# Optimization experiments

Hardware: AMD Instinct MI355X
Metric: run time of the kernel (lower is better)

Reference implementation:

```python
import jax, jax.numpy as jnp
import numpy as np

B, N, D, H, E = 4, 1024, 1024, 2048, 8

def setup_inputs() -> dict:
    key = jax.random.key(0)
    ks = jax.random.split(key, 5)
    return {
        "x": jax.random.normal(ks[0], (B, N, D), dtype=jnp.float32),
        "gate_w": jax.random.normal(ks[1], (D, E), dtype=jnp.float32) * 0.02,
        "gate_b": jnp.zeros((E,), dtype=jnp.float32),
        "w1": jax.random.normal(ks[2], (E, D, H), dtype=jnp.float32) * 0.02,
        "b1": jnp.zeros((E, H), dtype=jnp.float32),
        "w2": jax.random.normal(ks[3], (E, H, D), dtype=jnp.float32) * 0.02,
        "b2": jnp.zeros((E, D), dtype=jnp.float32),
        "gamma": jnp.ones((D,), dtype=jnp.float32),
    }

def reference(x, gate_w, gate_b, w1, b1, w2, b2, gamma):
    b, n, d = x.shape
    e = w1.shape[0]
    xf = x.reshape(b * n, d)                                    # [T, D]
    # gate: softmax over experts, then top-1
    probs = jax.nn.softmax(xf @ gate_w + gate_b, axis=-1)       # [T, E]
    top_val = jnp.max(probs, axis=-1, keepdims=True)            # [T, 1]
    top_idx = jnp.argmax(probs, axis=-1)                        # [T]
    # all-expert FFN (dense reference for masked dispatch; dropout in eval)
    h = jax.nn.gelu(jnp.einsum('td,edh->eth', xf, w1) + b1[:, None, :],
                    approximate=False)                          # [E, T, H]
    eo = jnp.einsum('eth,ehd->etd', h, w2) + b2[:, None, :]     # [E, T, D]
    onehot = jax.nn.one_hot(top_idx, e, dtype=xf.dtype)         # [T, E]
    out = jnp.einsum('etd,te->td', eo, onehot)                  # select routed expert
    y = (xf + out * top_val).reshape(b, n, d)
    # RMSNorm: F.normalize (L2, eps=1e-12) * gamma * sqrt(dim)
    nrm = jnp.linalg.norm(y, axis=-1, keepdims=True)
    y = y / jnp.maximum(nrm, 1e-12) * gamma * np.float32(np.sqrt(d))
    # load-balancing loss (unbiased variance like torch.var)
    importance = probs.sum(axis=0)                              # [E]
    load_loss = jnp.var(importance, ddof=1) / (jnp.mean(importance) ** 2 + 1e-10)
    return jax.nn.gelu(y, approximate=False), load_loss
```

## Files before the change

### kernel.cpp

```cpp
#include <hip/hip_runtime.h>
#include <math.h>

#define T_TOK 4096
#define DIM   1024
#define HID   2048
#define NE    8
#define TMM   128
#define TNN   128
#define BK    64
#define GATE_BLOCKS (T_TOK / 4)

typedef unsigned int  u32;
typedef unsigned short u16;
typedef __attribute__((ext_vector_type(8))) short bf16x8;
typedef __attribute__((ext_vector_type(4))) float f32x4;

__device__ __forceinline__ float gelu_exact(float v) {
    return 0.5f * v * (1.0f + erff(v * 0.70710678118654752440f));
}

__device__ __forceinline__ float gelu_fast(float x) {
    float u = 1.5957691216057308f * (x + 0.044715f * x * x * x);
    float e = __expf(u);
    float t = 1.f - 2.f / (e + 1.f);
    return 0.5f * x * (1.f + t);
}

__device__ __forceinline__ u16 f2bf(float v) {
    u32 u = __float_as_uint(v);
    u32 r = (u + 0x7FFFu + ((u >> 16) & 1u)) >> 16;
    return (u16)r;
}

__device__ __forceinline__ void gld_lds16(const void* g, void* l) {
    __builtin_amdgcn_global_load_lds(
        (const __attribute__((address_space(1))) u32*)g,
        (__attribute__((address_space(3))) u32*)l,
        16, 0, 0);
}

__global__ __launch_bounds__(256) void gate_kernel(
    const float* __restrict__ x, const float* __restrict__ gw,
    const float* __restrict__ gb, float* __restrict__ top_val,
    int* __restrict__ top_idx, float* __restrict__ partial_imp,
    int* __restrict__ partial_cnt)
{
    __shared__ float s_imp[NE];
    __shared__ int   s_cnt[NE];
    if (threadIdx.x < NE) { s_imp[threadIdx.x] = 0.f; s_cnt[threadIdx.x] = 0; }
    __syncthreads();

    const int wave = threadIdx.x >> 6;
    const int lane = threadIdx.x & 63;
    const int t = blockIdx.x * 4 + wave;

    float acc[NE];
    #pragma unroll
    for (int e = 0; e < NE; e++) acc[e] = 0.f;

    const float* xr = x + (size_t)t * DIM;
    #pragma unroll 4
    for (int k = lane; k < DIM; k += 64) {
        float xv = xr[k];
        const float* g = gw + (size_t)k * NE;
        float4 g0 = *(const float4*)g;
        float4 g1 = *(const float4*)(g + 4);
        acc[0] += xv * g0.x; acc[1] += xv * g0.y;
        acc[2] += xv * g0.z; acc[3] += xv * g0.w;
        acc[4] += xv * g1.x; acc[5] += xv * g1.y;
        acc[6] += xv * g1.z; acc[7] += xv * g1.w;
    }
    #pragma unroll
    for (int e = 0; e < NE; e++) {
        #pragma unroll
        for (int off = 32; off > 0; off >>= 1)
            acc[e] += __shfl_down(acc[e], off, 64);
    }
    if (lane == 0) {
        float l[NE];
        float m = -1e30f;
        #pragma unroll
        for (int e = 0; e < NE; e++) { l[e] = acc[e] + gb[e]; m = fmaxf(m, l[e]); }
        float s = 0.f;
        #pragma unroll
        for (int e = 0; e < NE; e++) { l[e] = expf(l[e] - m); s += l[e]; }
        float inv = 1.f / s;
        int bi = 0; float bv = -1.f;
        #pragma unroll
        for (int e = 0; e < NE; e++) {
            float p = l[e] * inv;
            atomicAdd(&s_imp[e], p);
            if (p > bv) { bv = p; bi = e; }
        }
        top_val[t] = bv;
        top_idx[t] = bi;
        atomicAdd(&s_cnt[bi], 1);
    }
    __syncthreads();
    if (threadIdx.x < NE) {
        partial_imp[blockIdx.x * NE + threadIdx.x] = s_imp[threadIdx.x];
        partial_cnt[blockIdx.x * NE + threadIdx.x] = s_cnt[threadIdx.x];
    }
}

__global__ __launch_bounds__(256) void plan_kernel(
    const float* __restrict__ partial_imp, const int* __restrict__ partial_cnt,
    int* __restrict__ counts, int* __restrict__ offsets,
    int* __restrict__ tile_e, int* __restrict__ tile_s,
    int* __restrict__ tile_rows, int* __restrict__ ntiles,
    float* __restrict__ loss_out)
{
    __shared__ float rimp[32][NE];
    __shared__ int   rcnt[32][NE];
    const int th = threadIdx.x;
    const int e = th & 7, chunk = th >> 3;
    float si = 0.f; int sc = 0;
    #pragma unroll 8
    for (int i = 0; i < GATE_BLOCKS / 32; i++) {
        const int b = chunk * (GATE_BLOCKS / 32) + i;
        si += partial_imp[b * NE + e];
        sc += partial_cnt[b * NE + e];
    }
    rimp[chunk][e] = si;
    rcnt[chunk][e] = sc;
    __syncthreads();
    if (th < NE) {
        float s = 0.f; int c = 0;
        for (int i = 0; i < 32; i++) { s += rimp[i][th]; c += rcnt[i][th]; }
        counts[th] = c;
        rimp[0][th] = s;
        rcnt[0][th] = c;
    }
    __syncthreads();
    if (th == 0) {
        int off = 0, nt = 0;
        for (int ee = 0; ee < NE; ee++) {
            offsets[ee] = off;
            const int c = rcnt[0][ee];
            for (int s = 0; s < c; s += TMM) {
                tile_e[nt] = ee;
                tile_s[nt] = off + s;
                tile_rows[nt] = min(TMM, c - s);
                nt++;
            }
            off += c;
        }
        offsets[NE] = off;
        *ntiles = nt;

        float mean = 0.f;
        for (int ee = 0; ee < NE; ee++) mean += rimp[0][ee];
        mean *= (1.0f / NE);
        float var = 0.f;
        for (int ee = 0; ee < NE; ee++) { float d = rimp[0][ee] - mean; var += d * d; }
        var *= (1.0f / (NE - 1));
        loss_out[0] = var / (mean * mean + 1e-10f);
    }
}

__global__ __launch_bounds__(256) void scatter_kernel(
    const int* __restrict__ top_idx, const int* __restrict__ offsets,
    int* __restrict__ cursors, int* __restrict__ sorted_tok)
{
    __shared__ int lcnt[NE], lbase[NE];
    if (threadIdx.x < NE) lcnt[threadIdx.x] = 0;
    __syncthreads();
    const int t = blockIdx.x * blockDim.x + threadIdx.x;
    const int e = top_idx[t];
    const int lrank = atomicAdd(&lcnt[e], 1);
    __syncthreads();
    if (threadIdx.x < NE)
        lbase[threadIdx.x] = atomicAdd(&cursors[threadIdx.x], lcnt[threadIdx.x]);
    __syncthreads();
    sorted_tok[offsets[e] + lbase[e] + lrank] = t;
}

__global__ __launch_bounds__(256) void gather_x_kernel(
    const float* __restrict__ x, const int* __restrict__ sorted_tok,
    u16* __restrict__ xs)
{
    const int s = blockIdx.x;
    const int tok = sorted_tok[s];
    const float* src = x + (size_t)tok * DIM;
    u16* dst = xs + (size_t)s * DIM;
    const int i = threadIdx.x * 4;
    float4 v = *(const float4*)&src[i];
    ushort4 o;
    o.x = f2bf(v.x); o.y = f2bf(v.y); o.z = f2bf(v.z); o.w = f2bf(v.w);
    *(ushort4*)&dst[i] = o;
}

__global__ __launch_bounds__(256) void transpose_bf16_kernel(
    const float* __restrict__ in, u16* __restrict__ out, int R, int C)
{
    __shared__ float tile[64][65];
    const float* src = in  + (size_t)blockIdx.z * R * C;
    u16*         dst = out + (size_t)blockIdx.z * R * C;
    const int c0 = blockIdx.x * 64, r0 = blockIdx.y * 64;
    const int th = threadIdx.x;

    const int tr  = th >> 4;
    const int tc4 = (th & 15) * 4;
    #pragma unroll
    for (int i = 0; i < 4; i++) {
        const int r = tr + i * 16;
        float4 v = *(const float4*)&src[(size_t)(r0 + r) * C + c0 + tc4];
        tile[r][tc4 + 0] = v.x; tile[r][tc4 + 1] = v.y;
        tile[r][tc4 + 2] = v.z; tile[r][tc4 + 3] = v.w;
    }
    __syncthreads();
    const int cc  = th >> 4;
    const int rr4 = (th & 15) * 4;
    #pragma unroll
    for (int i = 0; i < 4; i++) {
        const int c = cc + i * 16;
        ushort4 o;
        o.x = f2bf(tile[rr4 + 0][c]);
        o.y = f2bf(tile[rr4 + 1][c]);
        o.z = f2bf(tile[rr4 + 2][c]);
        o.w = f2bf(tile[rr4 + 3][c]);
        *(ushort4*)&dst[(size_t)(c0 + c) * R + r0 + rr4] = o;
    }
}

__global__ __launch_bounds__(256) void ffn1_mfma(
    const u16* __restrict__ xs, const u16* __restrict__ w1t,
    const float* __restrict__ b1,
    const int* __restrict__ tile_e, const int* __restrict__ tile_s,
    const int* __restrict__ tile_rows, const int* __restrict__ ntiles,
    u16* __restrict__ h_buf)
{
    const int tile = blockIdx.x;
    if (tile >= *ntiles) return;
    const int e     = tile_e[tile];
    const int sbase = tile_s[tile];
    const int rows  = tile_rows[tile];
    const int nbase = blockIdx.y * TNN;

    __shared__ __align__(16) u16 As[TMM * BK];
    __shared__ __align__(16) u16 Bs[TNN * BK];

    const int th = threadIdx.x;
    const int w  = th >> 6;
    const int l  = th & 63;
    const int wm = w >> 1, wn = w & 1;
    const int lr = l >> 3;
    const int lcs = ((l & 7) ^ lr) * 8;

    const u16* aptr[4];
    #pragma unroll
    for (int c = 0; c < 4; c++) {
        int srow = sbase + w * 32 + c * 8 + lr;
        if (srow > T_TOK - 1) srow = T_TOK - 1;
        aptr[c] = xs + (size_t)srow * DIM + lcs;
    }
    const u16* wb = w1t + (size_t)e * HID * DIM + (size_t)nbase * DIM;
    const u16* bptr[4];
    #pragma unroll
    for (int c = 0; c < 4; c++)
        bptr[c] = wb + (size_t)(w * 32 + c * 8 + lr) * DIM + lcs;

    f32x4 acc[4][4] = {};

    for (int k0 = 0; k0 < DIM; k0 += BK) {
        __syncthreads();
        #pragma unroll
        for (int c = 0; c < 4; c++)
            gld_lds16(aptr[c] + k0, &As[(w * 32 + c * 8) * BK]);
        #pragma unroll
        for (int c = 0; c < 4; c++)
            gld_lds16(bptr[c] + k0, &Bs[(w * 32 + c * 8) * BK]);
        __syncthreads();
        #pragma unroll
        for (int ks = 0; ks < 2; ks++) {
            const int ko = ((ks * 4 + (l >> 4)) ^ (l & 7)) * 8;
            bf16x8 af[4], bfr[4];
            #pragma unroll
            for (int i = 0; i < 4; i++)
                af[i]  = *(const bf16x8*)&As[(wm * 64 + i * 16 + (l & 15)) * BK + ko];
            #pragma unroll
            for (int i = 0; i < 4; i++)
                bfr[i] = *(const bf16x8*)&Bs[(wn * 64 + i * 16 + (l & 15)) * BK + ko];
            #pragma unroll
            for (int mi = 0; mi < 4; mi++)
                #pragma unroll
                for (int ni = 0; ni < 4; ni++)
                    acc[mi][ni] = __builtin_amdgcn_mfma_f32_16x16x32_bf16(
                        af[mi], bfr[ni], acc[mi][ni], 0, 0, 0);
        }
    }

    const int col = l & 15, quad = l >> 4;
    #pragma unroll
    for (int ni = 0; ni < 4; ni++) {
        const int n = nbase + wn * 64 + ni * 16 + col;
        const float bias = b1[e * HID + n];
        #pragma unroll
        for (int mi = 0; mi < 4; mi++) {
            #pragma unroll
            for (int r = 0; r < 4; r++) {
                const int m = wm * 64 + mi * 16 + quad * 4 + r;
                if (m < rows) {
                    float v = acc[mi][ni][r] + bias;
                    h_buf[(size_t)(sbase + m) * HID + n] = f2bf(gelu_fast(v));
                }
            }
        }
    }
}

__global__ __launch_bounds__(256) void ffn2_mfma(
    const u16* __restrict__ h_buf, const u16* __restrict__ w2t,
    const float* __restrict__ b2, const float* __restrict__ x,
    const int* __restrict__ sorted_tok, const float* __restrict__ top_val,
    const int* __restrict__ tile_e, const int* __restrict__ tile_s,
    const int* __restrict__ tile_rows, const int* __restrict__ ntiles,
    float* __restrict__ yout)
{
    const int tile = blockIdx.x;
    if (tile >= *ntiles) return;
    const int e     = tile_e[tile];
    const int sbase = tile_s[tile];
    const int rows  = tile_rows[tile];
    const int nbase = blockIdx.y * TNN;

    __shared__ __align__(16) u16 As[TMM * BK];
    __shared__ __align__(16) u16 Bs[TNN * BK];

    const int th = threadIdx.x;
    const int w  = th >> 6;
    const int l  = th & 63;
    const int wm = w >> 1, wn = w & 1;
    const int lr = l >> 3;
    const int lcs = ((l & 7) ^ lr) * 8;

    const u16* aptr[4];
    #pragma unroll
    for (int c = 0; c < 4; c++) {
        int srow = sbase + w * 32 + c * 8 + lr;
        if (srow > T_TOK - 1) srow = T_TOK - 1;
        aptr[c] = h_buf + (size_t)srow * HID + lcs;
    }
    const u16* wb = w2t + (size_t)e * DIM * HID + (size_t)nbase * HID;
    const u16* bptr[4];
    #pragma unroll
    for (int c = 0; c < 4; c++)
        bptr[c] = wb + (size_t)(w * 32 + c * 8 + lr) * HID + lcs;

    f32x4 acc[4][4] = {};

    for (int k0 = 0; k0 < HID; k0 += BK) {
        __syncthreads();
        #pragma unroll
        for (int c = 0; c < 4; c++)
            gld_lds16(aptr[c] + k0, &As[(w * 32 + c * 8) * BK]);
        #pragma unroll
        for (int c = 0; c < 4; c++)
            gld_lds16(bptr[c] + k0, &Bs[(w * 32 + c * 8) * BK]);
        __syncthreads();
        #pragma unroll
        for (int ks = 0; ks < 2; ks++) {
            const int ko = ((ks * 4 + (l >> 4)) ^ (l & 7)) * 8;
            bf16x8 af[4], bfr[4];
            #pragma unroll
            for (int i = 0; i < 4; i++)
                af[i]  = *(const bf16x8*)&As[(wm * 64 + i * 16 + (l & 15)) * BK + ko];
            #pragma unroll
            for (int i = 0; i < 4; i++)
                bfr[i] = *(const bf16x8*)&Bs[(wn * 64 + i * 16 + (l & 15)) * BK + ko];
            #pragma unroll
            for (int mi = 0; mi < 4; mi++)
                #pragma unroll
                for (int ni = 0; ni < 4; ni++)
                    acc[mi][ni] = __builtin_amdgcn_mfma_f32_16x16x32_bf16(
                        af[mi], bfr[ni], acc[mi][ni], 0, 0, 0);
        }
    }

    const int col = l & 15, quad = l >> 4;
    float bias[4];
    #pragma unroll
    for (int ni = 0; ni < 4; ni++)
        bias[ni] = b2[e * DIM + nbase + wn * 64 + ni * 16 + col];

    #pragma unroll
    for (int mi = 0; mi < 4; mi++) {
        #pragma unroll
        for (int r = 0; r < 4; r++) {
            const int m = wm * 64 + mi * 16 + quad * 4 + r;
            if (m < rows) {
                const int t = sorted_tok[sbase + m];
                const float tv = top_val[t];
                #pragma unroll
                for (int ni = 0; ni < 4; ni++) {
                    const int n = nbase + wn * 64 + ni * 16 + col;
                    float v = acc[mi][ni][r] + bias[ni];
                    yout[(size_t)t * DIM + n] = x[(size_t)t * DIM + n] + v * tv;
                }
            }
        }
    }
}

__global__ __launch_bounds__(256) void norm_kernel(float* __restrict__ y,
                                                   const float* __restrict__ gamma)
{
    const int t = blockIdx.x;
    float* row = y + (size_t)t * DIM;
    const int th = threadIdx.x;
    float4 v = *(const float4*)&row[th * 4];
    float ss = v.x * v.x + v.y * v.y + v.z * v.z + v.w * v.w;

    const int lane = th & 63, wave = th >> 6;
    #pragma unroll
    for (int off = 32; off > 0; off >>= 1) ss += __shfl_down(ss, off, 64);
    __shared__ float red[4];
    if (lane == 0) red[wave] = ss;
    __syncthreads();
    float total = red[0] + red[1] + red[2] + red[3];

    float nrm = sqrtf(total);
    float scale = 32.0f / fmaxf(nrm, 1e-12f);

    float4 g = *(const float4*)&gamma[th * 4];
    float4 o;
    o.x = gelu_exact(v.x * scale * g.x);
    o.y = gelu_exact(v.y * scale * g.y);
    o.z = gelu_exact(v.z * scale * g.z);
    o.w = gelu_exact(v.w * scale * g.w);
    *(float4*)&row[th * 4] = o;
}

extern "C" void kernel_launch(void* const* d_in, const int* in_sizes, int n_in,
                              void* d_out, int out_size, void* d_ws, size_t ws_size,
                              hipStream_t stream) {
    const float* x      = (const float*)d_in[0];
    const float* gate_w = (const float*)d_in[1];
    const float* gate_b = (const float*)d_in[2];
    const float* w1     = (const float*)d_in[3];
    const float* b1     = (const float*)d_in[4];
    const float* w2     = (const float*)d_in[5];
    const float* b2     = (const float*)d_in[6];
    const float* gamma  = (const float*)d_in[7];

    float* out  = (float*)d_out;
    float* loss = out + (size_t)T_TOK * DIM;

    char* ws = (char*)d_ws;
    float* top_val     = (float*)(ws + 0);
    int*   top_idx     = (int*)  (ws + 16384);
    int*   sorted_tok  = (int*)  (ws + 32768);
    int*   counts      = (int*)  (ws + 49152);
    int*   cursors     = (int*)  (ws + 49216);
    int*   offsets     = (int*)  (ws + 49280);
    int*   tile_e      = (int*)  (ws + 49664);
    int*   tile_s      = (int*)  (ws + 50176);
    int*   tile_rows   = (int*)  (ws + 50688);
    int*   ntiles      = (int*)  (ws + 51200);
    float* partial_imp = (float*)(ws + 65536);
    int*   partial_cnt = (int*)  (ws + 98304);
    u16*   x_sorted    = (u16*)  (ws + 131072);
    u16*   h_buf       = (u16*)  (ws + 131072 + 8388608);
    u16*   w1t         = (u16*)  (ws + 131072 + 8388608 + 16777216);
    u16*   w2t         = (u16*)  (ws + 131072 + 8388608 + 16777216 + 33554432);

    hipMemsetAsync(ws + 49216, 0, 64, stream);

    gate_kernel<<<GATE_BLOCKS, 256, 0, stream>>>(x, gate_w, gate_b, top_val,
                                                 top_idx, partial_imp,
                                                 partial_cnt);
    plan_kernel<<<1, 256, 0, stream>>>(partial_imp, partial_cnt, counts,
                                       offsets, tile_e, tile_s, tile_rows,
                                       ntiles, loss);
    scatter_kernel<<<T_TOK / 256, 256, 0, stream>>>(top_idx, offsets, cursors,
                                                    sorted_tok);
    gather_x_kernel<<<T_TOK, 256, 0, stream>>>(x, sorted_tok, x_sorted);
    transpose_bf16_kernel<<<dim3(HID / 64, DIM / 64, NE), 256, 0, stream>>>(
        w1, w1t, DIM, HID);
    transpose_bf16_kernel<<<dim3(DIM / 64, HID / 64, NE), 256, 0, stream>>>(
        w2, w2t, HID, DIM);

    ffn1_mfma<<<dim3(40, HID / TNN), 256, 0, stream>>>(
        x_sorted, w1t, b1, tile_e, tile_s, tile_rows, ntiles, h_buf);
    ffn2_mfma<<<dim3(40, DIM / TNN), 256, 0, stream>>>(
        h_buf, w2t, b2, x, sorted_tok, top_val, tile_e, tile_s, tile_rows,
        ntiles, out);
    norm_kernel<<<T_TOK, 256, 0, stream>>>(out, gamma);
}
```

Baseline: 320.6 us.

## Fuse weight transposes into gate kernel and widen FFN1 tiles to 128x256

Merges the two weight-transpose kernels and the gate kernel into one prep launch, so independent work shares a single grid and two launches go away. FFN1 now uses 512-thread blocks covering 256 output columns, doubling reuse of the A tile per load. Both FFN grids are reordered so blockIdx.x walks N tiles and blockIdx.y walks token tiles, which groups blocks that share the same expert weights and activations in time. The larger FFN1 block uses more LDS and registers per block, which may lower occupancy.

```diff
diff --git a/kernel.cpp b/kernel.cpp
--- a/kernel.cpp
+++ b/kernel.cpp
@@ -6,7 +6,6 @@
 #define HID   2048
 #define NE    8
 #define TMM   128
-#define TNN   128
 #define BK    64
 #define GATE_BLOCKS (T_TOK / 4)
 
@@ -39,20 +38,69 @@
         16, 0, 0);
 }
 
-__global__ __launch_bounds__(256) void gate_kernel(
+__device__ __forceinline__ void transpose_body(
+    const float* __restrict__ in, u16* __restrict__ out, int R, int C,
+    int bx, int by, int bz, float (*tile)[65])
+{
+    const float* src = in  + (size_t)bz * R * C;
+    u16*         dst = out + (size_t)bz * R * C;
+    const int c0 = bx * 64, r0 = by * 64;
+    const int th = threadIdx.x;
+
+    const int tr  = th >> 4;
+    const int tc4 = (th & 15) * 4;
+    #pragma unroll
+    for (int i = 0; i < 4; i++) {
+        const int r = tr + i * 16;
+        float4 v = *(const float4*)&src[(size_t)(r0 + r) * C + c0 + tc4];
+        tile[r][tc4 + 0] = v.x; tile[r][tc4 + 1] = v.y;
+        tile[r][tc4 + 2] = v.z; tile[r][tc4 + 3] = v.w;
+    }
+    __syncthreads();
+    const int cc  = th >> 4;
+    const int rr4 = (th & 15) * 4;
+    #pragma unroll
+    for (int i = 0; i < 4; i++) {
+        const int c = cc + i * 16;
+        ushort4 o;
+        o.x = f2bf(tile[rr4 + 0][c]);
+        o.y = f2bf(tile[rr4 + 1][c]);
+        o.z = f2bf(tile[rr4 + 2][c]);
+        o.w = f2bf(tile[rr4 + 3][c]);
+        *(ushort4*)&dst[(size_t)(c0 + c) * R + r0 + rr4] = o;
+    }
+}
+
+__global__ __launch_bounds__(256) void prep_kernel(
+    const float* __restrict__ w1, const float* __restrict__ w2,
+    u16* __restrict__ w1t, u16* __restrict__ w2t,
     const float* __restrict__ x, const float* __restrict__ gw,
     const float* __restrict__ gb, float* __restrict__ top_val,
     int* __restrict__ top_idx, float* __restrict__ partial_imp,
     int* __restrict__ partial_cnt)
 {
+    __shared__ float tile[64][65];
     __shared__ float s_imp[NE];
     __shared__ int   s_cnt[NE];
+
+    const int id = blockIdx.x;
+    if (id < 4096) {
+        transpose_body(w1, w1t, DIM, HID, id & 31, (id >> 5) & 15, id >> 9, tile);
+        return;
+    }
+    if (id < 8192) {
+        const int i2 = id - 4096;
+        transpose_body(w2, w2t, HID, DIM, i2 & 15, (i2 >> 4) & 31, i2 >> 9, tile);
+        return;
+    }
+
+    const int g = id - 8192;
     if (threadIdx.x < NE) { s_imp[threadIdx.x] = 0.f; s_cnt[threadIdx.x] = 0; }
     __syncthreads();
 
     const int wave = threadIdx.x >> 6;
     const int lane = threadIdx.x & 63;
-    const int t = blockIdx.x * 4 + wave;
+    const int t = g * 4 + wave;
 
     float acc[NE];
     #pragma unroll
@@ -62,9 +110,9 @@
     #pragma unroll 4
     for (int k = lane; k < DIM; k += 64) {
         float xv = xr[k];
-        const float* g = gw + (size_t)k * NE;
-        float4 g0 = *(const float4*)g;
-        float4 g1 = *(const float4*)(g + 4);
+        const float* gp = gw + (size_t)k * NE;
+        float4 g0 = *(const float4*)gp;
+        float4 g1 = *(const float4*)(gp + 4);
         acc[0] += xv * g0.x; acc[1] += xv * g0.y;
         acc[2] += xv * g0.z; acc[3] += xv * g0.w;
         acc[4] += xv * g1.x; acc[5] += xv * g1.y;
@@ -98,8 +146,8 @@
     }
     __syncthreads();
     if (threadIdx.x < NE) {
-        partial_imp[blockIdx.x * NE + threadIdx.x] = s_imp[threadIdx.x];
-        partial_cnt[blockIdx.x * NE + threadIdx.x] = s_cnt[threadIdx.x];
+        partial_imp[g * NE + threadIdx.x] = s_imp[threadIdx.x];
+        partial_cnt[g * NE + threadIdx.x] = s_cnt[threadIdx.x];
     }
 }
 
@@ -190,67 +238,34 @@
     *(ushort4*)&dst[i] = o;
 }
 
-__global__ __launch_bounds__(256) void transpose_bf16_kernel(
-    const float* __restrict__ in, u16* __restrict__ out, int R, int C)
-{
-    __shared__ float tile[64][65];
-    const float* src = in  + (size_t)blockIdx.z * R * C;
-    u16*         dst = out + (size_t)blockIdx.z * R * C;
-    const int c0 = blockIdx.x * 64, r0 = blockIdx.y * 64;
-    const int th = threadIdx.x;
-
-    const int tr  = th >> 4;
-    const int tc4 = (th & 15) * 4;
-    #pragma unroll
-    for (int i = 0; i < 4; i++) {
-        const int r = tr + i * 16;
-        float4 v = *(const float4*)&src[(size_t)(r0 + r) * C + c0 + tc4];
-        tile[r][tc4 + 0] = v.x; tile[r][tc4 + 1] = v.y;
-        tile[r][tc4 + 2] = v.z; tile[r][tc4 + 3] = v.w;
-    }
-    __syncthreads();
-    const int cc  = th >> 4;
-    const int rr4 = (th & 15) * 4;
-    #pragma unroll
-    for (int i = 0; i < 4; i++) {
-        const int c = cc + i * 16;
-        ushort4 o;
-        o.x = f2bf(tile[rr4 + 0][c]);
-        o.y = f2bf(tile[rr4 + 1][c]);
-        o.z = f2bf(tile[rr4 + 2][c]);
-        o.w = f2bf(tile[rr4 + 3][c]);
-        *(ushort4*)&dst[(size_t)(c0 + c) * R + r0 + rr4] = o;
-    }
-}
-
-__global__ __launch_bounds__(256) void ffn1_mfma(
+__global__ __launch_bounds__(512, 4) void ffn1_mfma(
     const u16* __restrict__ xs, const u16* __restrict__ w1t,
     const float* __restrict__ b1,
     const int* __restrict__ tile_e, const int* __restrict__ tile_s,
     const int* __restrict__ tile_rows, const int* __restrict__ ntiles,
     u16* __restrict__ h_buf)
 {
-    const int tile = blockIdx.x;
+    const int tile = blockIdx.y;
     if (tile >= *ntiles) return;
     const int e     = tile_e[tile];
     const int sbase = tile_s[tile];
     const int rows  = tile_rows[tile];
-    const int nbase = blockIdx.y * TNN;
-
-    __shared__ __align__(16) u16 As[TMM * BK];
-    __shared__ __align__(16) u16 Bs[TNN * BK];
+    const int nbase = blockIdx.x * 256;
+
+    __shared__ __align__(16) u16 As[128 * BK];
+    __shared__ __align__(16) u16 Bs[256 * BK];
 
     const int th = threadIdx.x;
     const int w  = th >> 6;
     const int l  = th & 63;
-    const int wm = w >> 1, wn = w & 1;
+    const int wm = w >> 2, wn = w & 3;
     const int lr = l >> 3;
     const int lcs = ((l & 7) ^ lr) * 8;
 
-    const u16* aptr[4];
-    #pragma unroll
-    for (int c = 0; c < 4; c++) {
-        int srow = sbase + w * 32 + c * 8 + lr;
+    const u16* aptr[2];
+    #pragma unroll
+    for (int c = 0; c < 2; c++) {
+        int srow = sbase + c * 64 + w * 8 + lr;
         if (srow > T_TOK - 1) srow = T_TOK - 1;
         aptr[c] = xs + (size_t)srow * DIM + lcs;
     }
@@ -258,18 +273,18 @@
     const u16* bptr[4];
     #pragma unroll
     for (int c = 0; c < 4; c++)
-        bptr[c] = wb + (size_t)(w * 32 + c * 8 + lr) * DIM + lcs;
+        bptr[c] = wb + (size_t)(c * 64 + w * 8 + lr) * DIM + lcs;
 
     f32x4 acc[4][4] = {};
 
     for (int k0 = 0; k0 < DIM; k0 += BK) {
         __syncthreads();
         #pragma unroll
+        for (int c = 0; c < 2; c++)
+            gld_lds16(aptr[c] + k0, &As[(c * 64 + w * 8) * BK]);
+        #pragma unroll
         for (int c = 0; c < 4; c++)
-            gld_lds16(aptr[c] + k0, &As[(w * 32 + c * 8) * BK]);
-        #pragma unroll
-        for (int c = 0; c < 4; c++)
-            gld_lds16(bptr[c] + k0, &Bs[(w * 32 + c * 8) * BK]);
+            gld_lds16(bptr[c] + k0, &Bs[(c * 64 + w * 8) * BK]);
         __syncthreads();
         #pragma unroll
         for (int ks = 0; ks < 2; ks++) {
@@ -317,15 +332,15 @@
     const int* __restrict__ tile_rows, const int* __restrict__ ntiles,
     float* __restrict__ yout)
 {
-    const int tile = blockIdx.x;
+    const int tile = blockIdx.y;
     if (tile >= *ntiles) return;
     const int e     = tile_e[tile];
     const int sbase = tile_s[tile];
     const int rows  = tile_rows[tile];
-    const int nbase = blockIdx.y * TNN;
-
-    __shared__ __align__(16) u16 As[TMM * BK];
-    __shared__ __align__(16) u16 Bs[TNN * BK];
+    const int nbase = blockIdx.x * 128;
+
+    __shared__ __align__(16) u16 As[128 * BK];
+    __shared__ __align__(16) u16 Bs[128 * BK];
 
     const int th = threadIdx.x;
     const int w  = th >> 6;
@@ -466,23 +481,19 @@
 
     hipMemsetAsync(ws + 49216, 0, 64, stream);
 
-    gate_kernel<<<GATE_BLOCKS, 256, 0, stream>>>(x, gate_w, gate_b, top_val,
-                                                 top_idx, partial_imp,
-                                                 partial_cnt);
+    prep_kernel<<<8192 + GATE_BLOCKS, 256, 0, stream>>>(
+        w1, w2, w1t, w2t, x, gate_w, gate_b, top_val, top_idx,
+        partial_imp, partial_cnt);
     plan_kernel<<<1, 256, 0, stream>>>(partial_imp, partial_cnt, counts,
                                        offsets, tile_e, tile_s, tile_rows,
                                        ntiles, loss);
     scatter_kernel<<<T_TOK / 256, 256, 0, stream>>>(top_idx, offsets, cursors,
                                                     sorted_tok);
     gather_x_kernel<<<T_TOK, 256, 0, stream>>>(x, sorted_tok, x_sorted);
-    transpose_bf16_kernel<<<dim3(HID / 64, DIM / 64, NE), 256, 0, stream>>>(
-        w1, w1t, DIM, HID);
-    transpose_bf16_kernel<<<dim3(DIM / 64, HID / 64, NE), 256, 0, stream>>>(
-        w2, w2t, HID, DIM);
-
-    ffn1_mfma<<<dim3(40, HID / TNN), 256, 0, stream>>>(
+
+    ffn1_mfma<<<dim3(HID / 256, 40), 512, 0, stream>>>(
         x_sorted, w1t, b1, tile_e, tile_s, tile_rows, ntiles, h_buf);
-    ffn2_mfma<<<dim3(40, DIM / TNN), 256, 0, stream>>>(
+    ffn2_mfma<<<dim3(DIM / 128, 40), 256, 0, stream>>>(
         h_buf, w2t, b2, x, sorted_tok, top_val, tile_e, tile_s, tile_rows,
         ntiles, out);
     norm_kernel<<<T_TOK, 256, 0, stream>>>(out, gamma);
```

Result: faster. 300.3 us (-6.3%).
